# Performance work log

Measured on AMD Instinct MI355X. Metric: run time of the kernel, lower is better.

## Reference

```python
import jax, jax.numpy as jnp
import numpy as np

N_NODES = 4096
IN_FEAT = 256
N_HEADS = 8
N_HIDDEN = 64  # out_features // n_heads
NEG_SLOPE = 0.2
EDGE_PROB = 0.05


def setup_inputs() -> dict:
    key = jax.random.key(0)
    k1, k2, k3, k4 = jax.random.split(key, 4)
    h = jax.random.normal(k1, (N_NODES, IN_FEAT), dtype=jnp.float32)
    # binary adjacency mask [N, N, 1] (broadcast over heads), as in the torch asserts
    adj_mat = (jax.random.uniform(k2, (N_NODES, N_NODES, 1)) < EDGE_PROB).astype(jnp.float32)
    # nn.Linear(in_features, n_heads*n_hidden, bias=False) weight: [H*F, in]
    W = jax.random.normal(k3, (N_HEADS * N_HIDDEN, IN_FEAT), dtype=jnp.float32) / np.sqrt(IN_FEAT)
    # nn.Linear(2*n_hidden, 1, bias=False) weight, flattened: [2*F]
    a = jax.random.normal(k4, (2 * N_HIDDEN,), dtype=jnp.float32) / np.sqrt(2 * N_HIDDEN)
    return {"h": h, "adj_mat": adj_mat, "W": W, "a": a}


def reference(h, adj_mat, W, a):
    n = h.shape[0]
    # g: [N, H, F]
    g = (h @ W.T).reshape(n, N_HEADS, N_HIDDEN)
    # attn(cat[g_i, g_j]) == a_l . g_i + a_r . g_j  (linear, no bias)
    a_l = a[:N_HIDDEN]
    a_r = a[N_HIDDEN:]
    el = jnp.einsum('ihf,f->ih', g, a_l)  # [N, H]
    er = jnp.einsum('jhf,f->jh', g, a_r)  # [N, H]
    e = jax.nn.leaky_relu(el[:, None, :] + er[None, :, :], NEG_SLOPE)  # [N, N, H]
    # note: original multiplies scores by adjacency (not masked_fill)
    e = e * adj_mat  # adj broadcasts over heads
    att = jax.nn.softmax(e, axis=1)  # softmax over source nodes j
    # dropout is identity at eval (dropout_rate=0.0)
    out = jnp.einsum('ijh,jhf->ihf', att, g)  # [N, H, F]
    return out.reshape(n, N_HEADS * N_HIDDEN)
```

## Files before the change

### kernel.cpp

```cpp
#include <hip/hip_runtime.h>

#define N_NODES 4096
#define IN_FEAT 256
#define N_HEADS 8
#define N_HIDDEN 64
#define OUT_FEAT (N_HEADS * N_HIDDEN)
#define NEG_SLOPE 0.2f

typedef _Float16 half8 __attribute__((ext_vector_type(8)));
typedef float floatx4 __attribute__((ext_vector_type(4)));

__global__ __launch_bounds__(256) void zero_kern(float* __restrict__ out,
                                                 float* __restrict__ Zp) {
  const int g = blockIdx.x * 256 + threadIdx.x;
  *(float4*)(out + (size_t)g * 4) = make_float4(0.f, 0.f, 0.f, 0.f);
  if (blockIdx.x < 32) *(float4*)(Zp + (size_t)g * 4) = make_float4(0.f, 0.f, 0.f, 0.f);
}

__global__ __launch_bounds__(256) void produce(
    const float* __restrict__ H, const float* __restrict__ adj,
    const float* __restrict__ Wt, const float* __restrict__ a,
    _Float16* __restrict__ GT16, float* __restrict__ elT,
    float* __restrict__ eR1, float* __restrict__ eR2,
    unsigned long long* __restrict__ bits) {
  __shared__ _Float16 SM[4 * 64 * 64];
  const int t = threadIdx.x;
  const int bx = blockIdx.x, by = blockIdx.y;

  if (by >= 8) {
    const int c = bx * 8 + (by - 8);
    const size_t W0 = (size_t)c * 512;
    const int wv = t >> 6, lane = t & 63;
    for (int k0 = 0; k0 < 128; k0 += 8) {
      float v[8];
#pragma unroll
      for (int k = 0; k < 8; ++k)
        v[k] = adj[(W0 + wv * 128 + k0 + k) * 64 + lane];
#pragma unroll
      for (int k = 0; k < 8; ++k) {
        unsigned long long m = __ballot(v[k] != 0.f);
        if (lane == 0) bits[W0 + wv * 128 + k0 + k] = m;
      }
    }
    return;
  }

  _Float16* Ah = SM;
  _Float16* Al = SM + 4096;
  _Float16* Bh = SM + 8192;
  _Float16* Bl = SM + 12288;
  const int w = t >> 6, l = t & 63;
  const int n16 = l & 15, q = l >> 4;
  const int bi = bx, bo = by;
  const int m0 = bi * 64 + w * 16;

  floatx4 acc[4];
#pragma unroll
  for (int ct = 0; ct < 4; ++ct) acc[ct] = (floatx4)0.f;

  for (int kc = 0; kc < 4; ++kc) {
    if (kc) __syncthreads();
#pragma unroll
    for (int p = 0; p < 4; ++p) {
      const int idx = p * 256 + t;
      const int r = idx >> 4;
      const int c4 = (idx & 15) << 2;
      const int dst = r * 64 + ((((idx & 15) >> 1)) ^ (r & 7)) * 8 + (idx & 1) * 4;
      float4 hv = *(const float4*)(H + (size_t)(bi * 64 + r) * IN_FEAT + kc * 64 + c4);
      float4 wv = *(const float4*)(Wt + (size_t)(bo * 64 + r) * IN_FEAT + kc * 64 + c4);
      union { _Float16 h[4]; int2 d; } hh_, hl_, wh_, wl_;
      hh_.h[0] = (_Float16)hv.x; hh_.h[1] = (_Float16)hv.y;
      hh_.h[2] = (_Float16)hv.z; hh_.h[3] = (_Float16)hv.w;
      hl_.h[0] = (_Float16)(hv.x - (float)hh_.h[0]);
      hl_.h[1] = (_Float16)(hv.y - (float)hh_.h[1]);
      hl_.h[2] = (_Float16)(hv.z - (float)hh_.h[2]);
      hl_.h[3] = (_Float16)(hv.w - (float)hh_.h[3]);
      wh_.h[0] = (_Float16)wv.x; wh_.h[1] = (_Float16)wv.y;
      wh_.h[2] = (_Float16)wv.z; wh_.h[3] = (_Float16)wv.w;
      wl_.h[0] = (_Float16)(wv.x - (float)wh_.h[0]);
      wl_.h[1] = (_Float16)(wv.y - (float)wh_.h[1]);
      wl_.h[2] = (_Float16)(wv.z - (float)wh_.h[2]);
      wl_.h[3] = (_Float16)(wv.w - (float)wh_.h[3]);
      *(int2*)&Ah[dst] = hh_.d;
      *(int2*)&Al[dst] = hl_.d;
      *(int2*)&Bh[dst] = wh_.d;
      *(int2*)&Bl[dst] = wl_.d;
    }
    __syncthreads();
#pragma unroll
    for (int ks = 0; ks < 2; ++ks) {
      const int ao = (w * 16 + n16) * 64 + (((ks << 2) + q) ^ (n16 & 7)) * 8;
      half8 Afh = *(const half8*)&Ah[ao];
      half8 Afl = *(const half8*)&Al[ao];
#pragma unroll
      for (int ct = 0; ct < 4; ++ct) {
        const int bofs = (ct * 16 + n16) * 64 + (((ks << 2) + q) ^ (n16 & 7)) * 8;
        half8 Bfh = *(const half8*)&Bh[bofs];
        half8 Bfl = *(const half8*)&Bl[bofs];
        acc[ct] = __builtin_amdgcn_mfma_f32_16x16x32_f16(Afh, Bfh, acc[ct], 0, 0, 0);
        acc[ct] = __builtin_amdgcn_mfma_f32_16x16x32_f16(Afl, Bfh, acc[ct], 0, 0, 0);
        acc[ct] = __builtin_amdgcn_mfma_f32_16x16x32_f16(Afh, Bfl, acc[ct], 0, 0, 0);
      }
    }
  }

  float aLv[4], aRv[4];
#pragma unroll
  for (int ct = 0; ct < 4; ++ct) {
    aLv[ct] = a[ct * 16 + n16];
    aRv[ct] = a[64 + ct * 16 + n16];
  }
#pragma unroll
  for (int reg = 0; reg < 4; ++reg) {
    float sl = 0.f, sr = 0.f;
#pragma unroll
    for (int ct = 0; ct < 4; ++ct) {
      sl = fmaf(acc[ct][reg], aLv[ct], sl);
      sr = fmaf(acc[ct][reg], aRv[ct], sr);
    }
#pragma unroll
    for (int off = 1; off < 16; off <<= 1) {
      sl += __shfl_xor(sl, off);
      sr += __shfl_xor(sr, off);
    }
    if (n16 == 0) {
      const int rowi = m0 + q * 4 + reg;
      elT[(size_t)bo * N_NODES + rowi] = sl;
      eR1[(size_t)bo * N_NODES + rowi] = __expf(sr);
      eR2[(size_t)bo * N_NODES + rowi] = __expf(0.2f * sr);
    }
  }

  __syncthreads();
  _Float16* LG = SM;
#pragma unroll
  for (int ct = 0; ct < 4; ++ct)
#pragma unroll
    for (int reg = 0; reg < 4; ++reg)
      LG[(w * 16 + q * 4 + reg) * 72 + ct * 16 + n16] = (_Float16)acc[ct][reg];
  __syncthreads();
  {
    const int f = t >> 2, jq = t & 3;
    union { _Float16 hh[16]; int4 v[2]; } u;
#pragma unroll
    for (int k = 0; k < 16; ++k) u.hh[k] = LG[(jq * 16 + k) * 72 + f];
    _Float16* dst = GT16 + (size_t)(bo * 64 + f) * N_NODES + bi * 64 + jq * 16;
    *(int4*)dst = u.v[0];
    *(int4*)(dst + 8) = u.v[1];
  }
}

__global__ __launch_bounds__(256) void attn_v3(
    const unsigned long long* __restrict__ bits, const _Float16* __restrict__ GT16,
    const float* __restrict__ elT, const float* __restrict__ eR1,
    const float* __restrict__ eR2, float* __restrict__ out, float* __restrict__ Zp) {
  __shared__ _Float16 Gt[2][64 * 64];
  __shared__ float eRs1[2][64], eRs2[2][64];
  __shared__ unsigned long long bitsS[2][64];
  __shared__ float eL1s[64], eL2s[64], ethrs[64];

  const int t = threadIdx.x;
  const int ib = blockIdx.x, h = blockIdx.y, s = blockIdx.z;
  const int i0 = ib * 64;
  const int jb0 = s * 1024;
  const int w = t >> 6, l = t & 63, n16 = l & 15, q = l >> 4;

  auto stage = [&](int par, int step) {
    if (t < 64) {
      eRs1[par][t] = eR1[(size_t)h * N_NODES + jb0 + step * 64 + t];
    } else if (t < 128) {
      eRs2[par][t - 64] = eR2[(size_t)h * N_NODES + jb0 + step * 64 + (t - 64)];
    } else if (t < 192) {
      bitsS[par][t - 128] = bits[(size_t)(i0 + t - 128) * 64 + s * 16 + step];
    }
    const int sf = t >> 2, sseg = t & 3;
    const _Float16* src = GT16 + (size_t)(h * 64 + sf) * N_NODES + jb0 + step * 64 + sseg * 16;
    int4 v0 = *(const int4*)src;
    int4 v1 = *(const int4*)(src + 8);
    *(int4*)&Gt[par][sf * 64 + ((sseg * 2) ^ (sf & 7)) * 8] = v0;
    *(int4*)&Gt[par][sf * 64 + ((sseg * 2 + 1) ^ (sf & 7)) * 8] = v1;
  };

  if (t < 64) {
    float e = elT[(size_t)h * N_NODES + i0 + t];
    eL1s[t] = __expf(e);
    eL2s[t] = __expf(0.2f * e);
    ethrs[t] = __expf(-e);
  }
  stage(0, 0);
  __syncthreads();

  const float eL1 = eL1s[w * 16 + n16];
  const float eL2 = eL2s[w * 16 + n16];
  const float ethr = ethrs[w * 16 + n16];

  floatx4 acc[4];
#pragma unroll
  for (int ft = 0; ft < 4; ++ft) acc[ft] = (floatx4)0.f;
  float zacc = 0.f;

  int par = 0;
  for (int step = 0; step < 16; ++step) {
    if (step + 1 < 16) stage(par ^ 1, step + 1);
    const unsigned long long bv = bitsS[par][w * 16 + n16];
#pragma unroll
    for (int ks = 0; ks < 2; ++ks) {
      const int j8 = ks * 32 + q * 8;
      const unsigned byte = (unsigned)(bv >> j8) & 0xffu;
      float4 r1a = *(const float4*)&eRs1[par][j8];
      float4 r1b = *(const float4*)&eRs1[par][j8 + 4];
      float4 r2a = *(const float4*)&eRs2[par][j8];
      float4 r2b = *(const float4*)&eRs2[par][j8 + 4];
      float r1[8] = {r1a.x, r1a.y, r1a.z, r1a.w, r1b.x, r1b.y, r1b.z, r1b.w};
      float r2[8] = {r2a.x, r2a.y, r2a.z, r2a.w, r2b.x, r2b.y, r2b.z, r2b.w};
      half8 Af;
#pragma unroll
      for (int k = 0; k < 8; ++k) {
        const bool pos = r1[k] > ethr;
        const float pv = (pos ? eL1 : eL2) * (pos ? r1[k] : r2[k]);
        const float p = ((byte >> k) & 1u) ? pv : 1.0f;
        zacc += p;
        Af[k] = (_Float16)p;
      }
#pragma unroll
      for (int ft = 0; ft < 4; ++ft) {
        half8 Bf = *(const half8*)&Gt[par][(ft * 16 + n16) * 64 + ((ks * 4 + q) ^ (n16 & 7)) * 8];
        acc[ft] = __builtin_amdgcn_mfma_f32_16x16x32_f16(Af, Bf, acc[ft], 0, 0, 0);
      }
    }
    __syncthreads();
    par ^= 1;
  }

  zacc += __shfl_xor(zacc, 16);
  zacc += __shfl_xor(zacc, 32);
  if (q == 0) atomicAdd(Zp + (size_t)h * N_NODES + i0 + w * 16 + n16, zacc);

#pragma unroll
  for (int ft = 0; ft < 4; ++ft)
#pragma unroll
    for (int reg = 0; reg < 4; ++reg)
      atomicAdd(out + (size_t)(i0 + w * 16 + q * 4 + reg) * OUT_FEAT + h * 64 + ft * 16 + n16,
                acc[ft][reg]);
}

__global__ __launch_bounds__(256) void normalize(float* __restrict__ out,
                                                 const float* __restrict__ Zp) {
  const int o = (blockIdx.x * 256 + threadIdx.x) * 4;
  const int i = o >> 9, h = (o >> 6) & 7;
  const float iz = 1.f / Zp[(size_t)h * N_NODES + i];
  float4 v = *(float4*)(out + o);
  v.x *= iz; v.y *= iz; v.z *= iz; v.w *= iz;
  *(float4*)(out + o) = v;
}

extern "C" void kernel_launch(void* const* d_in, const int* in_sizes, int n_in,
                              void* d_out, int out_size, void* d_ws, size_t ws_size,
                              hipStream_t stream) {
  const float* h   = (const float*)d_in[0];
  const float* adj = (const float*)d_in[1];
  const float* W   = (const float*)d_in[2];
  const float* a   = (const float*)d_in[3];
  float* out = (float*)d_out;

  char* ws = (char*)d_ws;
  _Float16* GT16 = (_Float16*)ws;
  unsigned long long* bits = (unsigned long long*)(ws + 4u * 1024 * 1024);
  float* elT = (float*)(ws + 6u * 1024 * 1024);
  float* eR1 = (float*)(ws + 6u * 1024 * 1024 + 128 * 1024);
  float* eR2 = (float*)(ws + 6u * 1024 * 1024 + 256 * 1024);
  float* Zp  = (float*)(ws + 6u * 1024 * 1024 + 384 * 1024);

  zero_kern<<<dim3(2048), 256, 0, stream>>>(out, Zp);
  produce<<<dim3(64, 16), 256, 0, stream>>>(h, adj, W, a, GT16, elT, eR1, eR2, bits);
  attn_v3<<<dim3(64, 8, 4), 256, 0, stream>>>(bits, GT16, elT, eR1, eR2, out, Zp);
  normalize<<<dim3(2048), 256, 0, stream>>>(out, Zp);
}
```

Measured before the change: 176.7 us.

## Replace split-K atomics with in-block two-way reduction and fused normalization

Each attention block now covers all source nodes for its 64 rows and head using 512 threads, where two groups of four waves each handle half of the source range and combine their results through shared memory. This removes the zero-init kernel, the global float atomics on the output and row sums, and the separate normalization pass. The row sum is now produced by an extra MFMA against a ones vector, and the leaky-relu select is replaced by an fmax of the two exponential branches. The cost is fewer blocks (512 instead of 2048) with a longer serial loop over source tiles, which may lower occupancy and latency hiding.

```diff
diff --git a/kernel.cpp b/kernel.cpp
--- a/kernel.cpp
+++ b/kernel.cpp
@@ -9,13 +9,6 @@
 
 typedef _Float16 half8 __attribute__((ext_vector_type(8)));
 typedef float floatx4 __attribute__((ext_vector_type(4)));
-
-__global__ __launch_bounds__(256) void zero_kern(float* __restrict__ out,
-                                                 float* __restrict__ Zp) {
-  const int g = blockIdx.x * 256 + threadIdx.x;
-  *(float4*)(out + (size_t)g * 4) = make_float4(0.f, 0.f, 0.f, 0.f);
-  if (blockIdx.x < 32) *(float4*)(Zp + (size_t)g * 4) = make_float4(0.f, 0.f, 0.f, 0.f);
-}
 
 __global__ __launch_bounds__(256) void produce(
     const float* __restrict__ H, const float* __restrict__ adj,
@@ -150,108 +143,133 @@
   }
 }
 
-__global__ __launch_bounds__(256) void attn_v3(
+__global__ __launch_bounds__(512) void attn_v5(
     const unsigned long long* __restrict__ bits, const _Float16* __restrict__ GT16,
     const float* __restrict__ elT, const float* __restrict__ eR1,
-    const float* __restrict__ eR2, float* __restrict__ out, float* __restrict__ Zp) {
-  __shared__ _Float16 Gt[2][64 * 64];
-  __shared__ float eRs1[2][64], eRs2[2][64];
-  __shared__ unsigned long long bitsS[2][64];
-  __shared__ float eL1s[64], eL2s[64], ethrs[64];
+    const float* __restrict__ eR2, float* __restrict__ out) {
+  __shared__ __align__(16) unsigned char GtRaw[2][2][8192];
+  __shared__ float eRs1[2][2][64], eRs2[2][2][64];
+  __shared__ unsigned long long bitsS[2][2][64];
+  __shared__ float eL1s[64], eL2s[64];
+  __shared__ float ZBuf[2][64];
 
   const int t = threadIdx.x;
-  const int ib = blockIdx.x, h = blockIdx.y, s = blockIdx.z;
+  const int ib = blockIdx.x, h = blockIdx.y;
   const int i0 = ib * 64;
-  const int jb0 = s * 1024;
   const int w = t >> 6, l = t & 63, n16 = l & 15, q = l >> 4;
+  const int jh = w >> 2, rt = w & 3;
 
   auto stage = [&](int par, int step) {
-    if (t < 64) {
-      eRs1[par][t] = eR1[(size_t)h * N_NODES + jb0 + step * 64 + t];
-    } else if (t < 128) {
-      eRs2[par][t - 64] = eR2[(size_t)h * N_NODES + jb0 + step * 64 + (t - 64)];
-    } else if (t < 192) {
-      bitsS[par][t - 128] = bits[(size_t)(i0 + t - 128) * 64 + s * 16 + step];
-    }
-    const int sf = t >> 2, sseg = t & 3;
-    const _Float16* src = GT16 + (size_t)(h * 64 + sf) * N_NODES + jb0 + step * 64 + sseg * 16;
-    int4 v0 = *(const int4*)src;
-    int4 v1 = *(const int4*)(src + 8);
-    *(int4*)&Gt[par][sf * 64 + ((sseg * 2) ^ (sf & 7)) * 8] = v0;
-    *(int4*)&Gt[par][sf * 64 + ((sseg * 2 + 1) ^ (sf & 7)) * 8] = v1;
+    const int sf = t >> 3, sseg = t & 7;
+#pragma unroll
+    for (int g = 0; g < 2; ++g) {
+      const _Float16* src =
+          GT16 + (size_t)(h * 64 + sf) * N_NODES + g * 2048 + step * 64 + sseg * 8;
+      int4 v = *(const int4*)src;
+      *(int4*)&((_Float16*)GtRaw[g][par])[sf * 64 + (sseg ^ (sf & 7)) * 8] = v;
+    }
+    if (t < 128) {
+      eRs1[t >> 6][par][t & 63] =
+          eR1[(size_t)h * N_NODES + (t >> 6) * 2048 + step * 64 + (t & 63)];
+    } else if (t < 256) {
+      const int u = t - 128;
+      eRs2[u >> 6][par][u & 63] =
+          eR2[(size_t)h * N_NODES + (u >> 6) * 2048 + step * 64 + (u & 63)];
+    } else if (t < 384) {
+      const int u = t - 256;
+      bitsS[u >> 6][par][u & 63] =
+          bits[(size_t)(i0 + (u & 63)) * 64 + (u >> 6) * 32 + step];
+    }
   };
 
   if (t < 64) {
     float e = elT[(size_t)h * N_NODES + i0 + t];
     eL1s[t] = __expf(e);
     eL2s[t] = __expf(0.2f * e);
-    ethrs[t] = __expf(-e);
   }
   stage(0, 0);
   __syncthreads();
 
-  const float eL1 = eL1s[w * 16 + n16];
-  const float eL2 = eL2s[w * 16 + n16];
-  const float ethr = ethrs[w * 16 + n16];
+  const float eL1 = eL1s[rt * 16 + n16];
+  const float eL2 = eL2s[rt * 16 + n16];
+  half8 Bones;
+#pragma unroll
+  for (int k = 0; k < 8; ++k) Bones[k] = (n16 == 0) ? (_Float16)1.f : (_Float16)0.f;
 
   floatx4 acc[4];
 #pragma unroll
   for (int ft = 0; ft < 4; ++ft) acc[ft] = (floatx4)0.f;
-  float zacc = 0.f;
+  floatx4 acc5 = (floatx4)0.f;
 
   int par = 0;
-  for (int step = 0; step < 16; ++step) {
-    if (step + 1 < 16) stage(par ^ 1, step + 1);
-    const unsigned long long bv = bitsS[par][w * 16 + n16];
+  for (int step = 0; step < 32; ++step) {
+    if (step + 1 < 32) stage(par ^ 1, step + 1);
+    const unsigned long long bv = bitsS[jh][par][rt * 16 + n16];
+    const _Float16* gt = (const _Float16*)GtRaw[jh][par];
 #pragma unroll
     for (int ks = 0; ks < 2; ++ks) {
       const int j8 = ks * 32 + q * 8;
       const unsigned byte = (unsigned)(bv >> j8) & 0xffu;
-      float4 r1a = *(const float4*)&eRs1[par][j8];
-      float4 r1b = *(const float4*)&eRs1[par][j8 + 4];
-      float4 r2a = *(const float4*)&eRs2[par][j8];
-      float4 r2b = *(const float4*)&eRs2[par][j8 + 4];
+      float4 r1a = *(const float4*)&eRs1[jh][par][j8];
+      float4 r1b = *(const float4*)&eRs1[jh][par][j8 + 4];
+      float4 r2a = *(const float4*)&eRs2[jh][par][j8];
+      float4 r2b = *(const float4*)&eRs2[jh][par][j8 + 4];
       float r1[8] = {r1a.x, r1a.y, r1a.z, r1a.w, r1b.x, r1b.y, r1b.z, r1b.w};
       float r2[8] = {r2a.x, r2a.y, r2a.z, r2a.w, r2b.x, r2b.y, r2b.z, r2b.w};
       half8 Af;
 #pragma unroll
       for (int k = 0; k < 8; ++k) {
-        const bool pos = r1[k] > ethr;
-        const float pv = (pos ? eL1 : eL2) * (pos ? r1[k] : r2[k]);
+        const float pv = fmaxf(eL1 * r1[k], eL2 * r2[k]);
         const float p = ((byte >> k) & 1u) ? pv : 1.0f;
-        zacc += p;
         Af[k] = (_Float16)p;
       }
 #pragma unroll
       for (int ft = 0; ft < 4; ++ft) {
-        half8 Bf = *(const half8*)&Gt[par][(ft * 16 + n16) * 64 + ((ks * 4 + q) ^ (n16 & 7)) * 8];
+        half8 Bf = *(const half8*)&gt[(ft * 16 + n16) * 64 + (((ks << 2) + q) ^ (n16 & 7)) * 8];
         acc[ft] = __builtin_amdgcn_mfma_f32_16x16x32_f16(Af, Bf, acc[ft], 0, 0, 0);
       }
+      acc5 = __builtin_amdgcn_mfma_f32_16x16x32_f16(Af, Bones, acc5, 0, 0, 0);
     }
     __syncthreads();
     par ^= 1;
   }
 
-  zacc += __shfl_xor(zacc, 16);
-  zacc += __shfl_xor(zacc, 32);
-  if (q == 0) atomicAdd(Zp + (size_t)h * N_NODES + i0 + w * 16 + n16, zacc);
-
-#pragma unroll
-  for (int ft = 0; ft < 4; ++ft)
-#pragma unroll
-    for (int reg = 0; reg < 4; ++reg)
-      atomicAdd(out + (size_t)(i0 + w * 16 + q * 4 + reg) * OUT_FEAT + h * 64 + ft * 16 + n16,
-                acc[ft][reg]);
-}
-
-__global__ __launch_bounds__(256) void normalize(float* __restrict__ out,
-                                                 const float* __restrict__ Zp) {
-  const int o = (blockIdx.x * 256 + threadIdx.x) * 4;
-  const int i = o >> 9, h = (o >> 6) & 7;
-  const float iz = 1.f / Zp[(size_t)h * N_NODES + i];
-  float4 v = *(float4*)(out + o);
-  v.x *= iz; v.y *= iz; v.z *= iz; v.w *= iz;
-  *(float4*)(out + o) = v;
+  float* comb1 = (float*)GtRaw;
+  if (jh == 1) {
+#pragma unroll
+    for (int ft = 0; ft < 4; ++ft)
+#pragma unroll
+      for (int reg = 0; reg < 4; ++reg)
+        comb1[(rt * 16 + q * 4 + reg) * 68 + ft * 16 + n16] = acc[ft][reg];
+    if (n16 == 0) {
+#pragma unroll
+      for (int reg = 0; reg < 4; ++reg) ZBuf[0][rt * 16 + q * 4 + reg] = acc5[reg];
+    }
+  }
+  __syncthreads();
+  if (jh == 0) {
+#pragma unroll
+    for (int ft = 0; ft < 4; ++ft)
+#pragma unroll
+      for (int reg = 0; reg < 4; ++reg)
+        acc[ft][reg] += comb1[(rt * 16 + q * 4 + reg) * 68 + ft * 16 + n16];
+    if (n16 == 0) {
+#pragma unroll
+      for (int reg = 0; reg < 4; ++reg)
+        ZBuf[1][rt * 16 + q * 4 + reg] = acc5[reg] + ZBuf[0][rt * 16 + q * 4 + reg];
+    }
+  }
+  __syncthreads();
+  if (jh == 0) {
+#pragma unroll
+    for (int reg = 0; reg < 4; ++reg) {
+      const int row = rt * 16 + q * 4 + reg;
+      const float invz = 1.f / ZBuf[1][row];
+      float* op = out + (size_t)(i0 + row) * OUT_FEAT + h * 64;
+#pragma unroll
+      for (int ft = 0; ft < 4; ++ft) op[ft * 16 + n16] = acc[ft][reg] * invz;
+    }
+  }
 }
 
 extern "C" void kernel_launch(void* const* d_in, const int* in_sizes, int n_in,
@@ -269,10 +287,7 @@
   float* elT = (float*)(ws + 6u * 1024 * 1024);
   float* eR1 = (float*)(ws + 6u * 1024 * 1024 + 128 * 1024);
   float* eR2 = (float*)(ws + 6u * 1024 * 1024 + 256 * 1024);
-  float* Zp  = (float*)(ws + 6u * 1024 * 1024 + 384 * 1024);
-
-  zero_kern<<<dim3(2048), 256, 0, stream>>>(out, Zp);
+
   produce<<<dim3(64, 16), 256, 0, stream>>>(h, adj, W, a, GT16, elT, eR1, eR2, bits);
-  attn_v3<<<dim3(64, 8, 4), 256, 0, stream>>>(bits, GT16, elT, eR1, eR2, out, Zp);
-  normalize<<<dim3(2048), 256, 0, stream>>>(out, Zp);
+  attn_v5<<<dim3(64, 8), 512, 0, stream>>>(bits, GT16, elT, eR1, eR2, out);
 }
```

Measured after the change: 169.2 us. 1.04x faster.
